# Optimization experiments

Hardware: AMD Instinct MI355X
Metric: run time of the kernel (lower is better)

Reference implementation:

```python
import jax, jax.numpy as jnp
import numpy as np

_CLIP = 1e4

def _n2n(t):
    return jnp.nan_to_num(t, nan=0.0, posinf=_CLIP, neginf=-_CLIP)

def setup_inputs() -> dict:
    key = jax.random.key(0)
    ks = jax.random.split(key, 9)
    B, N, E, DH, DM = 4, 16384, 65536, 128, 64
    s = 0.05
    return {
        "x": jax.random.normal(ks[0], (B, N, 3), jnp.float32),
        "h": jax.random.normal(ks[1], (B, N, DH), jnp.float32),
        "edge_index": jax.random.randint(ks[2], (B, E, 2), 0, N, jnp.int64 if jax.config.jax_enable_x64 else jnp.int32),
        "pe_w1": jax.random.normal(ks[3], (2 * DH + 1, DM), jnp.float32) * s,
        "pe_b1": jnp.zeros((DM,), jnp.float32),
        "pe_w2": jax.random.normal(ks[4], (DM, DM), jnp.float32) * s,
        "pe_b2": jnp.zeros((DM,), jnp.float32),
        "px_w": jax.random.normal(ks[5], (DM, 1), jnp.float32) * s,
        "ph_w1": jax.random.normal(ks[6], (DH + DM, DH), jnp.float32) * s,
        "ph_b1": jnp.zeros((DH,), jnp.float32),
        "ph_w2": jax.random.normal(ks[7], (DH, DH), jnp.float32) * s,
        "ph_b2": jnp.zeros((DH,), jnp.float32),
    }

def reference(x, h, edge_index, pe_w1, pe_b1, pe_w2, pe_b2, px_w, ph_w1, ph_b1, ph_w2, ph_b2):
    B = x.shape[0]
    src = edge_index[:, :, 0]          # [B,E]
    dst = edge_index[:, :, 1]
    bidx = jnp.arange(B)[:, None]      # [B,1] for batched gather/scatter
    x_i = x[bidx, src]                 # [B,E,3]
    x_j = x[bidx, dst]
    h_i = h[bidx, src]                 # [B,E,DH]
    h_j = h[bidx, dst]
    diff = x_i - x_j
    dist2 = jnp.clip((diff ** 2).sum(-1, keepdims=True), 1e-12, None)  # [B,E,1]
    edge_input = _n2n(jnp.concatenate([h_i, h_j, dist2], axis=-1))
    # phi_e: Linear -> SiLU -> Linear -> SiLU
    m = jax.nn.silu(edge_input @ pe_w1 + pe_b1)
    m_ij = _n2n(jax.nn.silu(m @ pe_w2 + pe_b2))   # [B,E,DM]
    m_x = m_ij @ px_w                             # [B,E,1]
    direction = diff / (jnp.sqrt(dist2) + 1e-8)
    delta_x_ij = _n2n(m_x * direction)            # [B,E,3]
    delta_x = jnp.zeros_like(x).at[bidx, src].add(delta_x_ij)
    delta_h_msg = jnp.zeros((B, x.shape[1], m_ij.shape[-1]), h.dtype).at[bidx, src].add(m_ij)
    h_input = jnp.concatenate([h, delta_h_msg], axis=-1)
    h_new = h + jax.nn.silu(h_input @ ph_w1 + ph_b1) @ ph_w2 + ph_b2
    x_new = x + delta_x
    return _n2n(x_new), _n2n(h_new)
```

## Files before the change

### kernel.cpp

```cpp
#include <hip/hip_runtime.h>


typedef unsigned short ushort_t;
typedef __attribute__((ext_vector_type(8))) short bf16x8;
typedef __attribute__((ext_vector_type(4))) float f32x4;
typedef _Float16 h2 __attribute__((ext_vector_type(2)));

__device__ __forceinline__ float fast_rcp(float v) { return __builtin_amdgcn_rcpf(v); }
__device__ __forceinline__ float fast_silu(float v) { return v * fast_rcp(1.0f + __expf(-v)); }
__device__ __forceinline__ ushort_t f2bf(float f) {
    unsigned u = __float_as_uint(f);
    u += 0x7fffu + ((u >> 16) & 1u);
    return (ushort_t)(u >> 16);
}
__device__ __forceinline__ float bf2f(ushort_t b) {
    return __uint_as_float(((unsigned)b) << 16);
}
__device__ __forceinline__ h2 u2h2(unsigned u) {
    union { unsigned u; h2 h; } v; v.u = u; return v.h;
}

__global__ __launch_bounds__(256) void init_k(const float* __restrict__ pe_w1,
                                              const float* __restrict__ pe_w2,
                                              const float* __restrict__ ph_w1,
                                              const float* __restrict__ ph_w2,
                                              ushort_t* __restrict__ W1t,
                                              ushort_t* __restrict__ Wp1t,
                                              ushort_t* __restrict__ Wp2t,
                                              unsigned* __restrict__ w2h) {
    int g = blockIdx.x * 256 + threadIdx.x;
    if (g < 16384) {
        int c = g >> 7, k = g & 127;
        float v = (c < 64) ? pe_w1[k * 64 + c] : pe_w1[(128 + k) * 64 + (c - 64)];
        W1t[g] = f2bf(v);
    } else if (g < 40960) {
        int g2 = g - 16384;
        int n = g2 / 192, k = g2 - n * 192;
        Wp1t[g2] = f2bf(ph_w1[k * 128 + n]);
    } else if (g < 57344) {
        int g3 = g - 40960;
        int n = g3 >> 7, k = g3 & 127;
        Wp2t[g3] = f2bf(ph_w2[k * 128 + n]);
    } else if (g < 59392) {
        int g4 = g - 57344;
        int k2 = g4 >> 6, c = g4 & 63;
        union { unsigned u; _Float16 h[2]; } p;
        p.h[0] = (_Float16)pe_w2[(2 * k2) * 64 + c];
        p.h[1] = (_Float16)pe_w2[(2 * k2 + 1) * 64 + c];
        w2h[g4] = p.u;
    }
}

template <bool EMIT_BF16>
__global__ __launch_bounds__(512) void pgemm_scatter_k(const float* __restrict__ A0,
                                                       const ushort_t* __restrict__ Wt,
                                                       ushort_t* __restrict__ outP,
                                                       ushort_t* __restrict__ hbout,
                                                       const int* __restrict__ ei,
                                                       int* __restrict__ cursor,
                                                       int* __restrict__ elist) {
    __shared__ ushort_t Bs[16384];
    const int tid = threadIdx.x;

    if (blockIdx.x >= 512) {
        int e = (blockIdx.x - 512) * 512 + tid;
        int2 sd = ((const int2*)ei)[e];
        int b = e >> 16;
        int gi = (b << 14) + sd.x;
        int gj = (b << 14) + sd.y;
        int slot = atomicAdd(&cursor[gi], 1);
        if (slot < 64) elist[gi * 64 + slot] = gj;
        return;
    }

    const int m0 = blockIdx.x * 128;
    const int wave = tid >> 6;
    const int lane = tid & 63;
    const int lr = lane & 15;
    const int lq = lane >> 4;

#pragma unroll
    for (int i = 0; i < 4; i++) {
        int c = tid + i * 512;
        int n = c >> 4, kg = c & 15;
        *(uint4*)&Bs[kg * 1024 + n * 8] = *(const uint4*)(Wt + n * 128 + kg * 8);
    }
    __syncthreads();

    f32x4 acc[8];
#pragma unroll
    for (int nt = 0; nt < 8; nt++) { f32x4 z = {0.f,0.f,0.f,0.f}; acc[nt] = z; }

    for (int k0 = 0; k0 < 128; k0 += 32) {
        int row = m0 + wave * 16 + lr;
        const float* src = A0 + (size_t)row * 128 + k0 + lq * 8;
        float4 v0 = *(const float4*)src;
        float4 v1 = *(const float4*)(src + 4);
        union { ushort_t s[8]; bf16x8 v; uint4 u; } p;
        p.s[0] = f2bf(v0.x); p.s[1] = f2bf(v0.y);
        p.s[2] = f2bf(v0.z); p.s[3] = f2bf(v0.w);
        p.s[4] = f2bf(v1.x); p.s[5] = f2bf(v1.y);
        p.s[6] = f2bf(v1.z); p.s[7] = f2bf(v1.w);
        if (EMIT_BF16)
            *(uint4*)(hbout + (size_t)row * 128 + k0 + lq * 8) = p.u;
        bf16x8 af = p.v;
        bf16x8 bfr[8];
        int kg = (k0 >> 3) + lq;
#pragma unroll
        for (int nt = 0; nt < 8; nt++)
            bfr[nt] = *(const bf16x8*)&Bs[kg * 1024 + (nt * 16 + lr) * 8];
#pragma unroll
        for (int nt = 0; nt < 8; nt++)
            acc[nt] = __builtin_amdgcn_mfma_f32_16x16x32_bf16(af, bfr[nt], acc[nt], 0, 0, 0);
    }
#pragma unroll
    for (int nt = 0; nt < 8; nt++)
#pragma unroll
        for (int r = 0; r < 4; r++) {
            int row = m0 + wave * 16 + lq * 4 + r;
            int col = nt * 16 + lr;
            outP[(size_t)row * 128 + col] = f2bf(acc[nt][r]);
        }
}

__global__ __launch_bounds__(64, 4) void node_k(const float* __restrict__ x,
                                                const ushort_t* __restrict__ P,
                                                const int* __restrict__ cursor,
                                                const int* __restrict__ elist,
                                                const float* __restrict__ w1,
                                                const float* __restrict__ b1,
                                                const unsigned* __restrict__ w2h,
                                                const float* __restrict__ b2,
                                                const float* __restrict__ pxw,
                                                ushort_t* __restrict__ dh,
                                                float* __restrict__ outx) {
    const int n = blockIdx.x;
    const int lane = threadIdx.x;
    __shared__ __attribute__((aligned(16))) unsigned m_u[32];
    ushort_t* mh = (ushort_t*)m_u;

    const float w1r = w1[256 * 64 + lane];
    const float b2v = b2[lane];
    const float pxv = pxw[lane];
    const float Pib = bf2f(P[(size_t)n * 128 + lane]) + b1[lane];
    const float xi0 = x[n * 3 + 0];
    const float xi1 = x[n * 3 + 1];
    const float xi2 = x[n * 3 + 2];

    float dhacc = 0.0f;
    float dxp0 = 0.0f, dxp1 = 0.0f, dxp2 = 0.0f;
    const int dg = min(cursor[n], 64);
    const int base = n * 64;

    int gj0 = (dg > 0) ? elist[base] : 0;
    float Pj = bf2f(P[(size_t)gj0 * 128 + 64 + lane]);
    float xj0 = x[gj0 * 3 + 0];
    float xj1 = x[gj0 * 3 + 1];
    float xj2 = x[gj0 * 3 + 2];

    for (int t = 0; t < dg; t++) {
        int gjn = (t + 1 < dg) ? elist[base + t + 1] : 0;
        float Pjn = bf2f(P[(size_t)gjn * 128 + 64 + lane]);
        float xn0 = x[gjn * 3 + 0];
        float xn1 = x[gjn * 3 + 1];
        float xn2 = x[gjn * 3 + 2];

        float ddx = xi0 - xj0;
        float ddy = xi1 - xj1;
        float ddz = xi2 - xj2;
        float d2 = fmaxf(ddx * ddx + ddy * ddy + ddz * ddz, 1e-12f);
        float m = fast_silu(Pib + Pj + d2 * w1r);
        __builtin_amdgcn_wave_barrier();
        union { ushort_t s; _Float16 h; } mc;
        mc.h = (_Float16)m;
        mh[lane] = mc.s;
        __builtin_amdgcn_wave_barrier();
        float s0 = b2v, s1 = 0.0f, s2 = 0.0f, s3 = 0.0f;
#pragma unroll
        for (int q = 0; q < 8; q++) {
            uint4 mm = *(const uint4*)&m_u[q * 4];
            s0 = __builtin_amdgcn_fdot2(u2h2(mm.x), u2h2(w2h[(4 * q + 0) * 64 + lane]), s0, false);
            s1 = __builtin_amdgcn_fdot2(u2h2(mm.y), u2h2(w2h[(4 * q + 1) * 64 + lane]), s1, false);
            s2 = __builtin_amdgcn_fdot2(u2h2(mm.z), u2h2(w2h[(4 * q + 2) * 64 + lane]), s2, false);
            s3 = __builtin_amdgcn_fdot2(u2h2(mm.w), u2h2(w2h[(4 * q + 3) * 64 + lane]), s3, false);
        }
        __builtin_amdgcn_wave_barrier();
        float m2 = fast_silu((s0 + s1) + (s2 + s3));
        dhacc += m2;
        float c = m2 * pxv * fast_rcp(sqrtf(d2) + 1e-8f);
        dxp0 = fmaf(c, ddx, dxp0);
        dxp1 = fmaf(c, ddy, dxp1);
        dxp2 = fmaf(c, ddz, dxp2);

        Pj = Pjn; xj0 = xn0; xj1 = xn1; xj2 = xn2;
    }

    dh[(size_t)n * 64 + lane] = f2bf(dhacc);

    for (int off = 32; off; off >>= 1) {
        dxp0 += __shfl_down(dxp0, off);
        dxp1 += __shfl_down(dxp1, off);
        dxp2 += __shfl_down(dxp2, off);
    }
    if (lane == 0) {
        outx[n * 3 + 0] = xi0 + dxp0;
        outx[n * 3 + 1] = xi1 + dxp1;
        outx[n * 3 + 2] = xi2 + dxp2;
    }
}

template <bool USE_HB>
__global__ __launch_bounds__(512) void mlp_fused_k(const float* __restrict__ h,
                                                   const ushort_t* __restrict__ hb,
                                                   const ushort_t* __restrict__ dh,
                                                   const ushort_t* __restrict__ Wp1t,
                                                   const float* __restrict__ b1,
                                                   const ushort_t* __restrict__ Wp2t,
                                                   const float* __restrict__ b2,
                                                   float* __restrict__ outh) {
    __shared__ ushort_t Ws[24576];
    __shared__ ushort_t Ts[16384];
    const int tid = threadIdx.x;
    const int m0 = blockIdx.x * 128;
    const int wave = tid >> 6;
    const int lane = tid & 63;
    const int lr = lane & 15;
    const int lq = lane >> 4;

#pragma unroll
    for (int i = 0; i < 6; i++) {
        int c = tid + i * 512;
        int kg = c >> 7, n = c & 127;
        *(uint4*)&Ws[kg * 1024 + n * 8] = *(const uint4*)(Wp1t + (size_t)n * 192 + kg * 8);
    }
    __syncthreads();

    f32x4 acc[8];
#pragma unroll
    for (int nt = 0; nt < 8; nt++) { f32x4 z = {0.f,0.f,0.f,0.f}; acc[nt] = z; }

    for (int k0 = 0; k0 < 192; k0 += 32) {
        int row = m0 + wave * 16 + lr;
        int k = k0 + lq * 8;
        bf16x8 af;
        if (k >= 128) {
            af = *(const bf16x8*)&dh[(size_t)row * 64 + (k - 128)];
        } else if (USE_HB) {
            af = *(const bf16x8*)&hb[(size_t)row * 128 + k];
        } else {
            const float* src = h + (size_t)row * 128 + k;
            float4 v0 = *(const float4*)src;
            float4 v1 = *(const float4*)(src + 4);
            union { ushort_t s[8]; bf16x8 v; } p;
            p.s[0] = f2bf(v0.x); p.s[1] = f2bf(v0.y);
            p.s[2] = f2bf(v0.z); p.s[3] = f2bf(v0.w);
            p.s[4] = f2bf(v1.x); p.s[5] = f2bf(v1.y);
            p.s[6] = f2bf(v1.z); p.s[7] = f2bf(v1.w);
            af = p.v;
        }
        bf16x8 bfr[8];
        int kg = (k0 >> 3) + lq;
#pragma unroll
        for (int nt = 0; nt < 8; nt++)
            bfr[nt] = *(const bf16x8*)&Ws[kg * 1024 + (nt * 16 + lr) * 8];
#pragma unroll
        for (int nt = 0; nt < 8; nt++)
            acc[nt] = __builtin_amdgcn_mfma_f32_16x16x32_bf16(af, bfr[nt], acc[nt], 0, 0, 0);
    }
#pragma unroll
    for (int nt = 0; nt < 8; nt++)
#pragma unroll
        for (int r = 0; r < 4; r++) {
            int row = wave * 16 + lq * 4 + r;
            int col = nt * 16 + lr;
            Ts[(col >> 3) * 1024 + row * 8 + (col & 7)] =
                f2bf(fast_silu(acc[nt][r] + b1[col]));
        }
    __builtin_amdgcn_wave_barrier();

    __syncthreads();
#pragma unroll
    for (int i = 0; i < 4; i++) {
        int c = tid + i * 512;
        int kg = c >> 7, n = c & 127;
        *(uint4*)&Ws[kg * 1024 + n * 8] = *(const uint4*)(Wp2t + (size_t)n * 128 + kg * 8);
    }
    __syncthreads();

    f32x4 acc2[8];
#pragma unroll
    for (int nt = 0; nt < 8; nt++) { f32x4 z = {0.f,0.f,0.f,0.f}; acc2[nt] = z; }

    for (int k0 = 0; k0 < 128; k0 += 32) {
        int kg = (k0 >> 3) + lq;
        bf16x8 af = *(const bf16x8*)&Ts[kg * 1024 + (wave * 16 + lr) * 8];
        bf16x8 bfr[8];
#pragma unroll
        for (int nt = 0; nt < 8; nt++)
            bfr[nt] = *(const bf16x8*)&Ws[kg * 1024 + (nt * 16 + lr) * 8];
#pragma unroll
        for (int nt = 0; nt < 8; nt++)
            acc2[nt] = __builtin_amdgcn_mfma_f32_16x16x32_bf16(af, bfr[nt], acc2[nt], 0, 0, 0);
    }
#pragma unroll
    for (int nt = 0; nt < 8; nt++)
#pragma unroll
        for (int r = 0; r < 4; r++) {
            int row = m0 + wave * 16 + lq * 4 + r;
            int col = nt * 16 + lr;
            float v = acc2[nt][r] + b2[col];
            if (USE_HB) v += bf2f(hb[(size_t)row * 128 + col]);
            else        v += h[(size_t)row * 128 + col];
            outh[(size_t)row * 128 + col] = v;
        }
}

extern "C" void kernel_launch(void* const* d_in, const int* in_sizes, int n_in,
                              void* d_out, int out_size, void* d_ws, size_t ws_size,
                              hipStream_t stream) {
    const float* x     = (const float*)d_in[0];
    const float* h     = (const float*)d_in[1];
    const int*   ei    = (const int*)d_in[2];
    const float* pe_w1 = (const float*)d_in[3];
    const float* pe_b1 = (const float*)d_in[4];
    const float* pe_w2 = (const float*)d_in[5];
    const float* pe_b2 = (const float*)d_in[6];
    const float* px_w  = (const float*)d_in[7];
    const float* ph_w1 = (const float*)d_in[8];
    const float* ph_b1 = (const float*)d_in[9];
    const float* ph_w2 = (const float*)d_in[10];
    const float* ph_b2 = (const float*)d_in[11];

    float* outx = (float*)d_out;
    float* outh = (float*)d_out + 196608;

    ushort_t* P    = (ushort_t*)d_ws;
    ushort_t* dh   = P + (size_t)65536 * 128;
    int* cursor    = (int*)(dh + (size_t)65536 * 64);
    int* elist     = cursor + 65536;
    ushort_t* W1t  = (ushort_t*)(elist + (size_t)65536 * 64);
    ushort_t* Wp1t = W1t + 16384;
    ushort_t* Wp2t = Wp1t + 24576;
    unsigned* w2h  = (unsigned*)(Wp2t + 16384);
    ushort_t* hb   = (ushort_t*)(w2h + 4096);
    size_t need_hb = (size_t)((char*)(hb + (size_t)65536 * 128) - (char*)d_ws);
    const bool use_hb = ws_size >= need_hb;

    hipMemsetAsync(cursor, 0, 65536 * sizeof(int), stream);
    init_k<<<232, 256, 0, stream>>>(pe_w1, pe_w2, ph_w1, ph_w2,
                                    W1t, Wp1t, Wp2t, w2h);
    if (use_hb)
        pgemm_scatter_k<true><<<1024, 512, 0, stream>>>(h, W1t, P, hb,
                                                        ei, cursor, elist);
    else
        pgemm_scatter_k<false><<<1024, 512, 0, stream>>>(h, W1t, P, nullptr,
                                                         ei, cursor, elist);
    node_k<<<65536, 64, 0, stream>>>(x, P, cursor, elist,
                                     pe_w1, pe_b1, w2h, pe_b2, px_w,
                                     dh, outx);
    if (use_hb)
        mlp_fused_k<true><<<512, 512, 0, stream>>>(h, hb, dh, Wp1t, ph_b1,
                                                   Wp2t, ph_b2, outh);
    else
        mlp_fused_k<false><<<512, 512, 0, stream>>>(h, nullptr, dh, Wp1t, ph_b1,
                                                    Wp2t, ph_b2, outh);
}
```

Measured before the change: 191.8 us.

## Fold weight-prep kernel into GEMM/scatter launch and preload edge list per wave

Removes the separate init kernel: the GEMM blocks now convert and transpose pe_w1 into shared memory straight from fp32, and extra blocks in the same launch convert the other MLP weights. In the node kernel, each lane loads one edge-list entry up front and the loop broadcasts neighbor indices with readlane, replacing a serial per-iteration load. This cuts one launch and its dependency gap, and takes a dependent global load off the neighbor loop. The cost is that every GEMM block redoes the strided fp32 weight conversion.

```diff
diff --git a/kernel.cpp b/kernel.cpp
--- a/kernel.cpp
+++ b/kernel.cpp
@@ -20,47 +20,42 @@
     union { unsigned u; h2 h; } v; v.u = u; return v.h;
 }
 
-__global__ __launch_bounds__(256) void init_k(const float* __restrict__ pe_w1,
+template <bool EMIT_BF16>
+__global__ __launch_bounds__(512) void mega_k(const float* __restrict__ A0,
+                                              const float* __restrict__ pe_w1,
+                                              ushort_t* __restrict__ outP,
+                                              ushort_t* __restrict__ hbout,
+                                              const int* __restrict__ ei,
+                                              int* __restrict__ cursor,
+                                              int* __restrict__ elist,
                                               const float* __restrict__ pe_w2,
                                               const float* __restrict__ ph_w1,
                                               const float* __restrict__ ph_w2,
-                                              ushort_t* __restrict__ W1t,
                                               ushort_t* __restrict__ Wp1t,
                                               ushort_t* __restrict__ Wp2t,
                                               unsigned* __restrict__ w2h) {
-    int g = blockIdx.x * 256 + threadIdx.x;
-    if (g < 16384) {
-        int c = g >> 7, k = g & 127;
-        float v = (c < 64) ? pe_w1[k * 64 + c] : pe_w1[(128 + k) * 64 + (c - 64)];
-        W1t[g] = f2bf(v);
-    } else if (g < 40960) {
-        int g2 = g - 16384;
-        int n = g2 / 192, k = g2 - n * 192;
-        Wp1t[g2] = f2bf(ph_w1[k * 128 + n]);
-    } else if (g < 57344) {
-        int g3 = g - 40960;
-        int n = g3 >> 7, k = g3 & 127;
-        Wp2t[g3] = f2bf(ph_w2[k * 128 + n]);
-    } else if (g < 59392) {
-        int g4 = g - 57344;
-        int k2 = g4 >> 6, c = g4 & 63;
-        union { unsigned u; _Float16 h[2]; } p;
-        p.h[0] = (_Float16)pe_w2[(2 * k2) * 64 + c];
-        p.h[1] = (_Float16)pe_w2[(2 * k2 + 1) * 64 + c];
-        w2h[g4] = p.u;
-    }
-}
-
-template <bool EMIT_BF16>
-__global__ __launch_bounds__(512) void pgemm_scatter_k(const float* __restrict__ A0,
-                                                       const ushort_t* __restrict__ Wt,
-                                                       ushort_t* __restrict__ outP,
-                                                       ushort_t* __restrict__ hbout,
-                                                       const int* __restrict__ ei,
-                                                       int* __restrict__ cursor,
-                                                       int* __restrict__ elist) {
     __shared__ ushort_t Bs[16384];
     const int tid = threadIdx.x;
+
+    if (blockIdx.x >= 1024) {
+        int g = (blockIdx.x - 1024) * 512 + tid;
+        if (g < 24576) {
+            int n = g / 192, k = g - n * 192;
+            Wp1t[g] = f2bf(ph_w1[k * 128 + n]);
+        } else if (g < 40960) {
+            int g3 = g - 24576;
+            int n = g3 >> 7, k = g3 & 127;
+            Wp2t[g3] = f2bf(ph_w2[k * 128 + n]);
+        } else if (g < 43008) {
+            int g4 = g - 40960;
+            int k2 = g4 >> 6, c = g4 & 63;
+            union { unsigned u; _Float16 h[2]; } p;
+            p.h[0] = (_Float16)pe_w2[(2 * k2) * 64 + c];
+            p.h[1] = (_Float16)pe_w2[(2 * k2 + 1) * 64 + c];
+            w2h[g4] = p.u;
+        }
+        return;
+    }
 
     if (blockIdx.x >= 512) {
         int e = (blockIdx.x - 512) * 512 + tid;
@@ -83,7 +78,12 @@
     for (int i = 0; i < 4; i++) {
         int c = tid + i * 512;
         int n = c >> 4, kg = c & 15;
-        *(uint4*)&Bs[kg * 1024 + n * 8] = *(const uint4*)(Wt + n * 128 + kg * 8);
+        const float* src = (n < 64) ? (pe_w1 + n) : (pe_w1 + 128 * 64 + (n - 64));
+        union { ushort_t s[8]; uint4 u; } p;
+#pragma unroll
+        for (int j = 0; j < 8; j++)
+            p.s[j] = f2bf(src[(kg * 8 + j) * 64]);
+        *(uint4*)&Bs[kg * 1024 + n * 8] = p.u;
     }
     __syncthreads();
 
@@ -150,16 +150,18 @@
     float dhacc = 0.0f;
     float dxp0 = 0.0f, dxp1 = 0.0f, dxp2 = 0.0f;
     const int dg = min(cursor[n], 64);
-    const int base = n * 64;
-
-    int gj0 = (dg > 0) ? elist[base] : 0;
-    float Pj = bf2f(P[(size_t)gj0 * 128 + 64 + lane]);
-    float xj0 = x[gj0 * 3 + 0];
-    float xj1 = x[gj0 * 3 + 1];
-    float xj2 = x[gj0 * 3 + 2];
+
+    int gjv = 0;
+    if (lane < dg) gjv = elist[n * 64 + lane];
+
+    int gj = __builtin_amdgcn_readlane(gjv, 0);
+    float Pj = bf2f(P[(size_t)gj * 128 + 64 + lane]);
+    float xj0 = x[gj * 3 + 0];
+    float xj1 = x[gj * 3 + 1];
+    float xj2 = x[gj * 3 + 2];
 
     for (int t = 0; t < dg; t++) {
-        int gjn = (t + 1 < dg) ? elist[base + t + 1] : 0;
+        int gjn = __builtin_amdgcn_readlane(gjv, (t + 1) & 63);
         float Pjn = bf2f(P[(size_t)gjn * 128 + 64 + lane]);
         float xn0 = x[gjn * 3 + 0];
         float xn1 = x[gjn * 3 + 1];
@@ -347,14 +349,12 @@
     const bool use_hb = ws_size >= need_hb;
 
     hipMemsetAsync(cursor, 0, 65536 * sizeof(int), stream);
-    init_k<<<232, 256, 0, stream>>>(pe_w1, pe_w2, ph_w1, ph_w2,
-                                    W1t, Wp1t, Wp2t, w2h);
     if (use_hb)
-        pgemm_scatter_k<true><<<1024, 512, 0, stream>>>(h, W1t, P, hb,
-                                                        ei, cursor, elist);
+        mega_k<true><<<1108, 512, 0, stream>>>(h, pe_w1, P, hb, ei, cursor, elist,
+                                               pe_w2, ph_w1, ph_w2, Wp1t, Wp2t, w2h);
     else
-        pgemm_scatter_k<false><<<1024, 512, 0, stream>>>(h, W1t, P, nullptr,
-                                                         ei, cursor, elist);
+        mega_k<false><<<1108, 512, 0, stream>>>(h, pe_w1, P, nullptr, ei, cursor, elist,
+                                                pe_w2, ph_w1, ph_w2, Wp1t, Wp2t, w2h);
     node_k<<<65536, 64, 0, stream>>>(x, P, cursor, elist,
                                      pe_w1, pe_b1, w2h, pe_b2, px_w,
                                      dh, outx);
```

New measurement: 205.3 us. 1.07x slower.
